# Kernel optimization log

Hardware: AMD Instinct MI355X
Metric: run time of the kernel (lower is better)

The kernel has to match this reference:

```python
import jax, jax.numpy as jnp
import numpy as np
from jax import lax

B, N, S = 16, 8192, 512
BASE_K = 16
MS_K = (8, 16, 24)


def _fps(xyz, npoint):
    # farthest point sampling; xyz [B,N,3] -> indices [B,npoint]
    b, n, _ = xyz.shape
    def body(carry, _):
        dists, far = carry
        c = jnp.take_along_axis(xyz, far[:, None, None], axis=1)  # [B,1,3]
        d = jnp.sum((xyz - c) ** 2, -1)
        dists = jnp.minimum(dists, d)
        return (dists, jnp.argmax(dists, -1).astype(jnp.int32)), far
    init = (jnp.full((b, n), 1e10, xyz.dtype), jnp.zeros((b,), jnp.int32))
    _, idx = lax.scan(body, init, None, length=npoint)
    return idx.swapaxes(0, 1)  # [B,npoint]


def _sqdist(a, b):
    # a [B,S,3], b [B,N,3] -> squared distances [B,S,N] (same topk order as cdist)
    return (jnp.sum(a * a, -1)[:, :, None] + jnp.sum(b * b, -1)[:, None, :]
            - 2.0 * jnp.einsum('bsc,bnc->bsn', a, b))


def _gather(pts, idx):
    # pts [B,N,C], idx [B,S,K] -> [B,S,K,C]
    b = pts.shape[0]
    return pts[jnp.arange(b)[:, None, None], idx]


def setup_inputs():
    key = jax.random.key(0)
    ks = jax.random.split(key, 6)
    s = 0.05
    return {
        'l0_xyz': jax.random.normal(ks[0], (B, 3, N), jnp.float32),
        'l0_points': jax.random.normal(ks[1], (B, 3, N), jnp.float32),
        'sa_W1': jax.random.normal(ks[2], (64, 6), jnp.float32) * s,
        'sa_b1': jnp.zeros((64,), jnp.float32),
        'sa_W2': jax.random.normal(ks[3], (128, 64), jnp.float32) * s,
        'sa_b2': jnp.zeros((128,), jnp.float32),
        'ms_W1': jax.random.normal(ks[4], (3, 64, 3), jnp.float32) * s,
        'ms_b1': jnp.zeros((3, 64), jnp.float32),
        'ms_W2': jax.random.normal(ks[5], (3, 128, 64), jnp.float32) * s,
        'ms_b2': jnp.zeros((3, 128), jnp.float32),
    }


def reference(l0_xyz, l0_points, sa_W1, sa_b1, sa_W2, sa_b2, ms_W1, ms_b1, ms_W2, ms_b2):
    xyz = l0_xyz.swapaxes(1, 2)     # [B,N,3]
    pts = l0_points.swapaxes(1, 2)  # [B,N,3]
    # --- PointNet_SA_Module_KNN: FPS + KNN grouping + shared MLP + max-pool ---
    fps_idx = _fps(lax.stop_gradient(xyz), S)                         # [B,S]
    new_xyz = jnp.take_along_axis(xyz, fps_idx[:, :, None], axis=1)  # [B,S,3]
    d = _sqdist(lax.stop_gradient(new_xyz), lax.stop_gradient(xyz))  # [B,S,N]
    _, knn_idx = lax.top_k(-d, BASE_K)                                # [B,S,K]
    g_xyz = _gather(xyz, knn_idx) - new_xyz[:, :, None]               # [B,S,K,3]
    g_pts = _gather(pts, knn_idx)                                     # [B,S,K,3]
    feat = jnp.concatenate([g_xyz, g_pts], -1)                        # [B,S,K,6]
    h = jax.nn.relu(jnp.einsum('bskc,oc->bsko', feat, sa_W1) + sa_b1)
    h = jnp.einsum('bsko,po->bskp', h, sa_W2) + sa_b2
    base_feat = jnp.max(h, axis=2)                                    # [B,S,128]
    keypoints = new_xyz.swapaxes(1, 2)                                # [B,3,S]
    # --- multi-scale: no_grad cdist, per-scale topk + rel-coord MLP + max-pool ---
    dist = _sqdist(lax.stop_gradient(new_xyz), lax.stop_gradient(xyz))  # [B,S,N]
    feats = [base_feat.swapaxes(1, 2)]                                  # [B,128,S]
    for i, k in enumerate(MS_K):
        k_eff = min(k, N)
        _, idx = lax.top_k(-dist, k_eff)                                # [B,S,k]
        rel = _gather(xyz, idx) - new_xyz[:, :, None]                   # [B,S,k,3]
        h = jax.nn.relu(jnp.einsum('bskc,oc->bsko', rel, ms_W1[i]) + ms_b1[i])
        h = jnp.einsum('bsko,po->bskp', h, ms_W2[i]) + ms_b2[i]
        feats.append(jnp.max(h, axis=2).swapaxes(1, 2))                 # [B,128,S]
    return keypoints, jnp.concatenate(feats, axis=1)                    # [B,3,S],[B,512,S]
```

## Files before the change

### kernel.cpp

```cpp
#include <hip/hip_runtime.h>

#define BB 16
#define NN 8192
#define SS 512
#define N3 (3 * NN)
#define KD 14

typedef unsigned short u16;
typedef unsigned int u32;
typedef unsigned long long u64;
typedef float v2f __attribute__((ext_vector_type(2)));

__device__ __forceinline__ v2f pk_add(v2f a, v2f b) {
  v2f r;
  asm("v_pk_add_f32 %0, %1, %2" : "=v"(r) : "v"(a), "v"(b));
  return r;
}
__device__ __forceinline__ v2f pk_mul(v2f a, v2f b) {
  v2f r;
  asm("v_pk_mul_f32 %0, %1, %2" : "=v"(r) : "v"(a), "v"(b));
  return r;
}

template <int CTRL>
__device__ __forceinline__ float dpp_maxf(float x) {
  int m = __builtin_amdgcn_update_dpp(0, __float_as_int(x), CTRL, 0xf, 0xf, false);
  return fmaxf(x, __int_as_float(m));
}
template <int CTRL>
__device__ __forceinline__ u32 dpp_maxu(u32 x) {
  u32 m = (u32)__builtin_amdgcn_update_dpp(0, (int)x, CTRL, 0xf, 0xf, false);
  return (x > m) ? x : m;
}

__global__ __attribute__((amdgpu_flat_work_group_size(256, 256),
                          amdgpu_waves_per_eu(1, 1)))
void k_fps(const float* __restrict__ xyz, float* __restrict__ out_kp) {
  __shared__ float sxyz[NN * 3];
  __shared__ int sIdx[SS];
  __shared__ u64 rkey[2][4];
  int b = blockIdx.x, t = threadIdx.x;
  const float* base = xyz + b * N3;
  v2f px[16], py[16], pz[16], dm[16];
#pragma unroll
  for (int j = 0; j < 16; ++j) {
    int n0 = j * 512 + t, n1 = n0 + 256;
    px[j] = v2f{base[n0], base[n1]};
    py[j] = v2f{base[NN + n0], base[NN + n1]};
    pz[j] = v2f{base[2 * NN + n0], base[2 * NN + n1]};
    dm[j] = v2f{1e10f, 1e10f};
    sxyz[n0 * 3 + 0] = px[j].x;
    sxyz[n0 * 3 + 1] = py[j].x;
    sxyz[n0 * 3 + 2] = pz[j].x;
    sxyz[n1 * 3 + 0] = px[j].y;
    sxyz[n1 * 3 + 1] = py[j].y;
    sxyz[n1 * 3 + 2] = pz[j].y;
  }
#pragma unroll
  for (int j = 0; j < 16; ++j) {
    asm volatile("" : "+v"(px[j]), "+v"(py[j]), "+v"(pz[j]));
  }
  float cx = base[0], cy = base[NN], cz = base[2 * NN];
  int far = 0;
  int lane = t & 63, w = t >> 6;
  u32 tb = (u32)(NN - t);
  for (int it = 0; it < SS; ++it) {
    if (t == 0) sIdx[it] = far;
    v2f ncx = v2f{-cx, -cx}, ncy = v2f{-cy, -cy}, ncz = v2f{-cz, -cz};
    float vmax = 0.0f;
#pragma unroll
    for (int j = 0; j < 16; ++j) {
      v2f dx = pk_add(px[j], ncx);
      v2f dy = pk_add(py[j], ncy);
      v2f dz = pk_add(pz[j], ncz);
      v2f xx = pk_mul(dx, dx);
      v2f yy = pk_mul(dy, dy);
      v2f s = pk_add(xx, yy);
      v2f zz = pk_mul(dz, dz);
      v2f d = pk_add(s, zz);
      float a0 = fminf(dm[j].x, d.x);
      float a1 = fminf(dm[j].y, d.y);
      dm[j].x = a0;
      dm[j].y = a1;
      vmax = fmaxf(vmax, fmaxf(a0, a1));
    }
    vmax = dpp_maxf<0x111>(vmax);
    vmax = dpp_maxf<0x112>(vmax);
    vmax = dpp_maxf<0x114>(vmax);
    vmax = dpp_maxf<0x118>(vmax);
    vmax = dpp_maxf<0x142>(vmax);
    vmax = dpp_maxf<0x143>(vmax);
    float wv = __int_as_float(__builtin_amdgcn_readlane(__float_as_int(vmax), 63));
    u32 cand = 0;
#pragma unroll
    for (int j = 15; j >= 0; --j) {
      u32 v1 = tb - (u32)(j * 512 + 256);
      u32 v0 = tb - (u32)(j * 512);
      cand = (dm[j].y == wv) ? v1 : cand;
      cand = (dm[j].x == wv) ? v0 : cand;
    }
    cand = dpp_maxu<0x111>(cand);
    cand = dpp_maxu<0x112>(cand);
    cand = dpp_maxu<0x114>(cand);
    cand = dpp_maxu<0x118>(cand);
    cand = dpp_maxu<0x142>(cand);
    cand = dpp_maxu<0x143>(cand);
    int pb = it & 1;
    if (lane == 63) rkey[pb][w] = ((u64)__float_as_uint(wv) << 32) | cand;
    __syncthreads();
    u64 k0 = rkey[pb][0], k1 = rkey[pb][1];
    u64 k2 = rkey[pb][2], k3 = rkey[pb][3];
    u64 k01 = (k0 > k1) ? k0 : k1;
    u64 k23 = (k2 > k3) ? k2 : k3;
    u64 kg = (k01 > k23) ? k01 : k23;
    far = NN - (int)(u32)(kg & 0xffffffffu);
    cx = sxyz[far * 3 + 0];
    cy = sxyz[far * 3 + 1];
    cz = sxyz[far * 3 + 2];
  }
  __syncthreads();
  for (int i = t; i < SS; i += 256) {
    int id = sIdx[i];
    out_kp[b * 1536 + i] = base[id];
    out_kp[b * 1536 + SS + i] = base[NN + id];
    out_kp[b * 1536 + 2 * SS + i] = base[2 * NN + id];
  }
}

__global__ __launch_bounds__(256) void k_knn(const float* __restrict__ xyz,
                                             const float* __restrict__ kp,
                                             u16* __restrict__ knn) {
  int t = threadIdx.x;
  int row = blockIdx.x * 4 + (t >> 6);
  int lane = t & 63;
  int b = row >> 9, s = row & (SS - 1);
  const float* base = xyz + b * N3;
  float ax = kp[b * 1536 + s];
  float ay = kp[b * 1536 + SS + s];
  float az = kp[b * 1536 + 2 * SS + s];
  float aw = __fadd_rn(__fadd_rn(__fmul_rn(ax, ax), __fmul_rn(ay, ay)), __fmul_rn(az, az));
  u64 arr[KD];
#pragma unroll
  for (int i = 0; i < KD; ++i) arr[i] = ~0ull;
  for (int c = 0; c < 128; ++c) {
    int n = c * 64 + lane;
    float qx = base[n], qy = base[NN + n], qz = base[2 * NN + n];
    float qw = __fadd_rn(__fadd_rn(__fmul_rn(qx, qx), __fmul_rn(qy, qy)), __fmul_rn(qz, qz));
    float dot = __fadd_rn(__fadd_rn(__fmul_rn(ax, qx), __fmul_rn(ay, qy)), __fmul_rn(az, qz));
    float d = __fsub_rn(__fadd_rn(aw, qw), __fmul_rn(2.0f, dot));
    u32 ub = __float_as_uint(d);
    ub ^= (ub & 0x80000000u) ? 0xFFFFFFFFu : 0x80000000u;
    u64 key = ((u64)ub << 32) | (u32)n;
    if (key < arr[KD - 1]) {
#pragma unroll
      for (int i = KD - 1; i >= 1; --i) {
        u64 am = arr[i - 1];
        arr[i] = (am > key) ? am : ((arr[i] > key) ? key : arr[i]);
      }
      if (arr[0] > key) arr[0] = key;
    }
  }
  u64 mine = 0;
  for (int it = 0; it < 24; ++it) {
    u64 m = arr[0];
#pragma unroll
    for (int off = 1; off < 64; off <<= 1) {
      u64 o = __shfl_xor(m, off, 64);
      m = (o < m) ? o : m;
    }
    if (lane == it) mine = m;
    if (arr[0] == m) {
#pragma unroll
      for (int i = 0; i < KD - 1; ++i) arr[i] = arr[i + 1];
      arr[KD - 1] = ~0ull;
    }
  }
  if (lane < 24) knn[row * 24 + lane] = (u16)(mine & 0xFFFFu);
}

__global__ __launch_bounds__(256) void k_base(
    const float* __restrict__ xyz, const float* __restrict__ pts,
    const float* __restrict__ kp, const u16* __restrict__ knn,
    const float* __restrict__ W1, const float* __restrict__ b1,
    const float* __restrict__ W2, const float* __restrict__ b2,
    float* __restrict__ out) {
  __shared__ float sW1T[6 * 64];
  __shared__ float sb1[64];
  __shared__ float sfeat[4][16 * 6];
  __shared__ float sh1[4][16 * 64];
  int t = threadIdx.x, lane = t & 63, w = t >> 6;
  int b = blockIdx.x >> 6, s0 = (blockIdx.x & 63) * 8;
  for (int i = t; i < 384; i += 256) {
    int o = i / 6, c = i - o * 6;
    sW1T[c * 64 + o] = W1[i];
  }
  if (t < 64) sb1[t] = b1[t];
  float wgtA[64], wgtB[64];
#pragma unroll
  for (int j = 0; j < 64; ++j) {
    wgtA[j] = W2[lane * 64 + j];
    wgtB[j] = W2[(lane + 64) * 64 + j];
  }
  float b2A = b2[lane], b2B = b2[lane + 64];
  __syncthreads();
  for (int g = 0; g < 2; ++g) {
    for (int i = t; i < 384; i += 256) {
      int rr = i / 96, rem = i - rr * 96, k = rem / 6, c = rem - k * 6;
      int s = s0 + g * 4 + rr, row = b * SS + s;
      int id = knn[row * 24 + k];
      float val;
      if (c < 3) {
        val = __fsub_rn(xyz[b * N3 + c * NN + id], kp[b * 1536 + c * SS + s]);
      } else {
        val = pts[b * N3 + (c - 3) * NN + id];
      }
      sfeat[rr][k * 6 + c] = val;
    }
    __syncthreads();
#pragma unroll
    for (int m = 0; m < 16; ++m) {
      int u = m * 256 + t;
      int rr = u >> 10, rem = u & 1023, k = rem >> 6, o = rem & 63;
      float acc = sb1[o];
#pragma unroll
      for (int c = 0; c < 6; ++c) acc = fmaf(sfeat[rr][k * 6 + c], sW1T[c * 64 + o], acc);
      sh1[rr][k * 64 + o] = fmaxf(acc, 0.f);
    }
    __syncthreads();
    float bestA = -1e30f, bestB = -1e30f;
#pragma unroll
    for (int k = 0; k < 16; ++k) {
      const float4* h4 = (const float4*)&sh1[w][k * 64];
      float a0 = 0.f, a1 = 0.f;
#pragma unroll
      for (int j = 0; j < 16; ++j) {
        float4 hv = h4[j];
        a0 = fmaf(hv.x, wgtA[4 * j], a0);
        a0 = fmaf(hv.y, wgtA[4 * j + 1], a0);
        a0 = fmaf(hv.z, wgtA[4 * j + 2], a0);
        a0 = fmaf(hv.w, wgtA[4 * j + 3], a0);
        a1 = fmaf(hv.x, wgtB[4 * j], a1);
        a1 = fmaf(hv.y, wgtB[4 * j + 1], a1);
        a1 = fmaf(hv.z, wgtB[4 * j + 2], a1);
        a1 = fmaf(hv.w, wgtB[4 * j + 3], a1);
      }
      bestA = fmaxf(bestA, a0);
      bestB = fmaxf(bestB, a1);
    }
    int s = s0 + g * 4 + w;
    out[24576 + b * 262144 + lane * 512 + s] = bestA + b2A;
    out[24576 + b * 262144 + (lane + 64) * 512 + s] = bestB + b2B;
    __syncthreads();
  }
}

__global__ __launch_bounds__(256) void k_ms(
    const float* __restrict__ xyz, const float* __restrict__ kp,
    const u16* __restrict__ knn, const float* __restrict__ msW1,
    const float* __restrict__ msb1, const float* __restrict__ msW2,
    const float* __restrict__ msb2, float* __restrict__ out) {
  int scale = blockIdx.y;
  int kk = 8 * (scale + 1);
  __shared__ float sW1T[3 * 64];
  __shared__ float sb1[64];
  __shared__ float sfeat[4][24 * 3];
  __shared__ float sh1[4][24 * 64];
  int t = threadIdx.x, lane = t & 63, w = t >> 6;
  int b = blockIdx.x >> 6, s0 = (blockIdx.x & 63) * 8;
  const float* W1s = msW1 + scale * 192;
  for (int i = t; i < 192; i += 256) {
    int o = i / 3, c = i - o * 3;
    sW1T[c * 64 + o] = W1s[i];
  }
  if (t < 64) sb1[t] = msb1[scale * 64 + t];
  float wgtA[64], wgtB[64];
#pragma unroll
  for (int j = 0; j < 64; ++j) {
    wgtA[j] = msW2[scale * 8192 + lane * 64 + j];
    wgtB[j] = msW2[scale * 8192 + (lane + 64) * 64 + j];
  }
  float b2A = msb2[scale * 128 + lane], b2B = msb2[scale * 128 + lane + 64];
  __syncthreads();
  int co = 128 * (scale + 1);
  for (int g = 0; g < 2; ++g) {
    int nfeat = 4 * kk * 3;
    for (int i = t; i < nfeat; i += 256) {
      int kk3 = kk * 3;
      int rr = i / kk3, rem = i - rr * kk3, k = rem / 3, c = rem - k * 3;
      int s = s0 + g * 4 + rr, row = b * SS + s;
      int id = knn[row * 24 + k];
      sfeat[rr][k * 3 + c] = __fsub_rn(xyz[b * N3 + c * NN + id], kp[b * 1536 + c * SS + s]);
    }
    __syncthreads();
    for (int rr = 0; rr < 4; ++rr) {
      for (int u = t; u < kk * 64; u += 256) {
        int k = u >> 6, o = u & 63;
        float acc = sb1[o];
        acc = fmaf(sfeat[rr][k * 3 + 0], sW1T[o], acc);
        acc = fmaf(sfeat[rr][k * 3 + 1], sW1T[64 + o], acc);
        acc = fmaf(sfeat[rr][k * 3 + 2], sW1T[128 + o], acc);
        sh1[rr][k * 64 + o] = fmaxf(acc, 0.f);
      }
    }
    __syncthreads();
    float bestA = -1e30f, bestB = -1e30f;
    for (int k = 0; k < kk; ++k) {
      const float4* h4 = (const float4*)&sh1[w][k * 64];
      float a0 = 0.f, a1 = 0.f;
#pragma unroll
      for (int j = 0; j < 16; ++j) {
        float4 hv = h4[j];
        a0 = fmaf(hv.x, wgtA[4 * j], a0);
        a0 = fmaf(hv.y, wgtA[4 * j + 1], a0);
        a0 = fmaf(hv.z, wgtA[4 * j + 2], a0);
        a0 = fmaf(hv.w, wgtA[4 * j + 3], a0);
        a1 = fmaf(hv.x, wgtB[4 * j], a1);
        a1 = fmaf(hv.y, wgtB[4 * j + 1], a1);
        a1 = fmaf(hv.z, wgtB[4 * j + 2], a1);
        a1 = fmaf(hv.w, wgtB[4 * j + 3], a1);
      }
      bestA = fmaxf(bestA, a0);
      bestB = fmaxf(bestB, a1);
    }
    int s = s0 + g * 4 + w;
    out[24576 + b * 262144 + (co + lane) * 512 + s] = bestA + b2A;
    out[24576 + b * 262144 + (co + lane + 64) * 512 + s] = bestB + b2B;
    __syncthreads();
  }
}

extern "C" void kernel_launch(void* const* d_in, const int* in_sizes, int n_in,
                              void* d_out, int out_size, void* d_ws, size_t ws_size,
                              hipStream_t stream) {
  const float* xyz = (const float*)d_in[0];
  const float* pts = (const float*)d_in[1];
  const float* sa_W1 = (const float*)d_in[2];
  const float* sa_b1 = (const float*)d_in[3];
  const float* sa_W2 = (const float*)d_in[4];
  const float* sa_b2 = (const float*)d_in[5];
  const float* ms_W1 = (const float*)d_in[6];
  const float* ms_b1 = (const float*)d_in[7];
  const float* ms_W2 = (const float*)d_in[8];
  const float* ms_b2 = (const float*)d_in[9];
  float* out = (float*)d_out;
  const float* kp = (const float*)d_out;

  u16* knn = (u16*)d_ws;

  k_fps<<<BB, 256, 0, stream>>>(xyz, out);
  k_knn<<<(BB * SS) / 4, 256, 0, stream>>>(xyz, kp, knn);
  k_base<<<BB * 64, 256, 0, stream>>>(xyz, pts, kp, knn, sa_W1, sa_b1, sa_W2, sa_b2, out);
  k_ms<<<dim3(BB * 64, 3), 256, 0, stream>>>(xyz, kp, knn, ms_W1, ms_b1, ms_W2, ms_b2, out);
}
```

Baseline: 1.031 ms.

## Fuse KNN, base MLP and multi-scale MLP into one kernel with packed FMA

New measurement: 1.829 ms. +77.5%, slower.

```diff
diff --git a/kernel.cpp b/kernel.cpp
--- a/kernel.cpp
+++ b/kernel.cpp
@@ -19,6 +19,11 @@
 __device__ __forceinline__ v2f pk_mul(v2f a, v2f b) {
   v2f r;
   asm("v_pk_mul_f32 %0, %1, %2" : "=v"(r) : "v"(a), "v"(b));
+  return r;
+}
+__device__ __forceinline__ v2f pk_fma(v2f a, v2f b, v2f c) {
+  v2f r;
+  asm("v_pk_fma_f32 %0, %1, %2, %3" : "=v"(r) : "v"(a), "v"(b), "v"(c));
   return r;
 }
 
@@ -127,205 +132,182 @@
   }
 }
 
-__global__ __launch_bounds__(256) void k_knn(const float* __restrict__ xyz,
-                                             const float* __restrict__ kp,
-                                             u16* __restrict__ knn) {
-  int t = threadIdx.x;
-  int row = blockIdx.x * 4 + (t >> 6);
-  int lane = t & 63;
-  int b = row >> 9, s = row & (SS - 1);
-  const float* base = xyz + b * N3;
-  float ax = kp[b * 1536 + s];
-  float ay = kp[b * 1536 + SS + s];
-  float az = kp[b * 1536 + 2 * SS + s];
-  float aw = __fadd_rn(__fadd_rn(__fmul_rn(ax, ax), __fmul_rn(ay, ay)), __fmul_rn(az, az));
-  u64 arr[KD];
-#pragma unroll
-  for (int i = 0; i < KD; ++i) arr[i] = ~0ull;
-  for (int c = 0; c < 128; ++c) {
-    int n = c * 64 + lane;
-    float qx = base[n], qy = base[NN + n], qz = base[2 * NN + n];
-    float qw = __fadd_rn(__fadd_rn(__fmul_rn(qx, qx), __fmul_rn(qy, qy)), __fmul_rn(qz, qz));
-    float dot = __fadd_rn(__fadd_rn(__fmul_rn(ax, qx), __fmul_rn(ay, qy)), __fmul_rn(az, qz));
-    float d = __fsub_rn(__fadd_rn(aw, qw), __fmul_rn(2.0f, dot));
-    u32 ub = __float_as_uint(d);
-    ub ^= (ub & 0x80000000u) ? 0xFFFFFFFFu : 0x80000000u;
-    u64 key = ((u64)ub << 32) | (u32)n;
-    if (key < arr[KD - 1]) {
-#pragma unroll
-      for (int i = KD - 1; i >= 1; --i) {
-        u64 am = arr[i - 1];
-        arr[i] = (am > key) ? am : ((arr[i] > key) ? key : arr[i]);
-      }
-      if (arr[0] > key) arr[0] = key;
-    }
-  }
-  u64 mine = 0;
-  for (int it = 0; it < 24; ++it) {
-    u64 m = arr[0];
-#pragma unroll
-    for (int off = 1; off < 64; off <<= 1) {
-      u64 o = __shfl_xor(m, off, 64);
-      m = (o < m) ? o : m;
-    }
-    if (lane == it) mine = m;
-    if (arr[0] == m) {
-#pragma unroll
-      for (int i = 0; i < KD - 1; ++i) arr[i] = arr[i + 1];
-      arr[KD - 1] = ~0ull;
-    }
-  }
-  if (lane < 24) knn[row * 24 + lane] = (u16)(mine & 0xFFFFu);
-}
-
-__global__ __launch_bounds__(256) void k_base(
-    const float* __restrict__ xyz, const float* __restrict__ pts,
-    const float* __restrict__ kp, const u16* __restrict__ knn,
-    const float* __restrict__ W1, const float* __restrict__ b1,
-    const float* __restrict__ W2, const float* __restrict__ b2,
-    float* __restrict__ out) {
+__global__ __attribute__((amdgpu_flat_work_group_size(256, 256),
+                          amdgpu_waves_per_eu(1, 1)))
+void k_tail(const float* __restrict__ xyz, const float* __restrict__ pts,
+            const float* __restrict__ kp, const float* __restrict__ W1,
+            const float* __restrict__ b1, const float* __restrict__ W2,
+            const float* __restrict__ b2, const float* __restrict__ msW1,
+            const float* __restrict__ msb1, const float* __restrict__ msW2,
+            const float* __restrict__ msb2, float* __restrict__ out) {
+  __shared__ u16 sknn[4][24];
   __shared__ float sW1T[6 * 64];
   __shared__ float sb1[64];
+  __shared__ float sW1m[3 * 64];
+  __shared__ float sb1m[64];
   __shared__ float sfeat[4][16 * 6];
-  __shared__ float sh1[4][16 * 64];
+  __shared__ float sh1[4][24 * 64];
   int t = threadIdx.x, lane = t & 63, w = t >> 6;
-  int b = blockIdx.x >> 6, s0 = (blockIdx.x & 63) * 8;
+  int row0 = blockIdx.x * 4;
+  int b = row0 >> 9;
+  int s0 = row0 & (SS - 1);
+  const float* base = xyz + b * N3;
+  const float* kpb = kp + b * 1536;
+  float* outb = out + 24576 + b * 262144;
+
   for (int i = t; i < 384; i += 256) {
     int o = i / 6, c = i - o * 6;
     sW1T[c * 64 + o] = W1[i];
   }
   if (t < 64) sb1[t] = b1[t];
-  float wgtA[64], wgtB[64];
-#pragma unroll
-  for (int j = 0; j < 64; ++j) {
-    wgtA[j] = W2[lane * 64 + j];
-    wgtB[j] = W2[(lane + 64) * 64 + j];
-  }
-  float b2A = b2[lane], b2B = b2[lane + 64];
+
+  {
+    int s = s0 + w;
+    float ax = kpb[s], ay = kpb[SS + s], az = kpb[2 * SS + s];
+    float aw = __fadd_rn(__fadd_rn(__fmul_rn(ax, ax), __fmul_rn(ay, ay)),
+                         __fmul_rn(az, az));
+    u64 arr[KD];
+#pragma unroll
+    for (int i = 0; i < KD; ++i) arr[i] = ~0ull;
+    for (int c = 0; c < 128; ++c) {
+      int n = c * 64 + lane;
+      float qx = base[n], qy = base[NN + n], qz = base[2 * NN + n];
+      float qw = __fadd_rn(__fadd_rn(__fmul_rn(qx, qx), __fmul_rn(qy, qy)),
+                           __fmul_rn(qz, qz));
+      float dot = __fadd_rn(__fadd_rn(__fmul_rn(ax, qx), __fmul_rn(ay, qy)),
+                            __fmul_rn(az, qz));
+      float d = __fsub_rn(__fadd_rn(aw, qw), __fmul_rn(2.0f, dot));
+      u32 ub = __float_as_uint(d);
+      ub ^= (ub & 0x80000000u) ? 0xFFFFFFFFu : 0x80000000u;
+      u64 key = ((u64)ub << 32) | (u32)n;
+      if (key < arr[KD - 1]) {
+#pragma unroll
+        for (int i = KD - 1; i >= 1; --i) {
+          u64 am = arr[i - 1];
+          arr[i] = (am > key) ? am : ((arr[i] > key) ? key : arr[i]);
+        }
+        if (arr[0] > key) arr[0] = key;
+      }
+    }
+    for (int it = 0; it < 24; ++it) {
+      u64 m = arr[0];
+#pragma unroll
+      for (int off = 1; off < 64; off <<= 1) {
+        u64 o = __shfl_xor(m, off, 64);
+        m = (o < m) ? o : m;
+      }
+      if (lane == it) sknn[w][it] = (u16)(m & 0xFFFFu);
+      if (arr[0] == m) {
+#pragma unroll
+        for (int i = 0; i < KD - 1; ++i) arr[i] = arr[i + 1];
+        arr[KD - 1] = ~0ull;
+      }
+    }
+  }
   __syncthreads();
-  for (int g = 0; g < 2; ++g) {
-    for (int i = t; i < 384; i += 256) {
-      int rr = i / 96, rem = i - rr * 96, k = rem / 6, c = rem - k * 6;
-      int s = s0 + g * 4 + rr, row = b * SS + s;
-      int id = knn[row * 24 + k];
-      float val;
-      if (c < 3) {
-        val = __fsub_rn(xyz[b * N3 + c * NN + id], kp[b * 1536 + c * SS + s]);
-      } else {
-        val = pts[b * N3 + (c - 3) * NN + id];
-      }
-      sfeat[rr][k * 6 + c] = val;
-    }
+
+  for (int i = t; i < 384; i += 256) {
+    int rr = i / 96, rem = i - rr * 96, k = rem / 6, c = rem - k * 6;
+    int s = s0 + rr;
+    int id = sknn[rr][k];
+    float val;
+    if (c < 3) {
+      val = __fsub_rn(base[c * NN + id], kpb[c * SS + s]);
+    } else {
+      val = pts[b * N3 + (c - 3) * NN + id];
+    }
+    sfeat[rr][k * 6 + c] = val;
+  }
+  __syncthreads();
+#pragma unroll
+  for (int m = 0; m < 16; ++m) {
+    int u = m * 256 + t;
+    int rr = u >> 10, rem = u & 1023, k = rem >> 6, o = rem & 63;
+    float acc = sb1[o];
+#pragma unroll
+    for (int c = 0; c < 6; ++c) acc = fmaf(sfeat[rr][k * 6 + c], sW1T[c * 64 + o], acc);
+    sh1[rr][k * 64 + o] = fmaxf(acc, 0.f);
+  }
+  __syncthreads();
+  {
+    const v2f* W2v = (const v2f*)W2;
+    v2f wA[32], wB[32];
+#pragma unroll
+    for (int j = 0; j < 32; ++j) {
+      wA[j] = W2v[lane * 32 + j];
+      wB[j] = W2v[(lane + 64) * 32 + j];
+    }
+    float bestA = -1e30f, bestB = -1e30f;
+#pragma unroll
+    for (int k = 0; k < 16; ++k) {
+      const v2f* h2 = (const v2f*)&sh1[w][k * 64];
+      v2f aA = v2f{0.f, 0.f}, aB = v2f{0.f, 0.f};
+#pragma unroll
+      for (int j = 0; j < 32; ++j) {
+        v2f hv = h2[j];
+        aA = pk_fma(hv, wA[j], aA);
+        aB = pk_fma(hv, wB[j], aB);
+      }
+      bestA = fmaxf(bestA, aA.x + aA.y);
+      bestB = fmaxf(bestB, aB.x + aB.y);
+    }
+    int s = s0 + w;
+    outb[lane * 512 + s] = bestA + b2[lane];
+    outb[(lane + 64) * 512 + s] = bestB + b2[lane + 64];
+  }
+
+  for (int scale = 0; scale < 3; ++scale) {
+    int kk = 8 * (scale + 1);
     __syncthreads();
-#pragma unroll
-    for (int m = 0; m < 16; ++m) {
-      int u = m * 256 + t;
-      int rr = u >> 10, rem = u & 1023, k = rem >> 6, o = rem & 63;
-      float acc = sb1[o];
-#pragma unroll
-      for (int c = 0; c < 6; ++c) acc = fmaf(sfeat[rr][k * 6 + c], sW1T[c * 64 + o], acc);
-      sh1[rr][k * 64 + o] = fmaxf(acc, 0.f);
-    }
-    __syncthreads();
-    float bestA = -1e30f, bestB = -1e30f;
-#pragma unroll
-    for (int k = 0; k < 16; ++k) {
-      const float4* h4 = (const float4*)&sh1[w][k * 64];
-      float a0 = 0.f, a1 = 0.f;
-#pragma unroll
-      for (int j = 0; j < 16; ++j) {
-        float4 hv = h4[j];
-        a0 = fmaf(hv.x, wgtA[4 * j], a0);
-        a0 = fmaf(hv.y, wgtA[4 * j + 1], a0);
-        a0 = fmaf(hv.z, wgtA[4 * j + 2], a0);
-        a0 = fmaf(hv.w, wgtA[4 * j + 3], a0);
-        a1 = fmaf(hv.x, wgtB[4 * j], a1);
-        a1 = fmaf(hv.y, wgtB[4 * j + 1], a1);
-        a1 = fmaf(hv.z, wgtB[4 * j + 2], a1);
-        a1 = fmaf(hv.w, wgtB[4 * j + 3], a1);
-      }
-      bestA = fmaxf(bestA, a0);
-      bestB = fmaxf(bestB, a1);
-    }
-    int s = s0 + g * 4 + w;
-    out[24576 + b * 262144 + lane * 512 + s] = bestA + b2A;
-    out[24576 + b * 262144 + (lane + 64) * 512 + s] = bestB + b2B;
-    __syncthreads();
-  }
-}
-
-__global__ __launch_bounds__(256) void k_ms(
-    const float* __restrict__ xyz, const float* __restrict__ kp,
-    const u16* __restrict__ knn, const float* __restrict__ msW1,
-    const float* __restrict__ msb1, const float* __restrict__ msW2,
-    const float* __restrict__ msb2, float* __restrict__ out) {
-  int scale = blockIdx.y;
-  int kk = 8 * (scale + 1);
-  __shared__ float sW1T[3 * 64];
-  __shared__ float sb1[64];
-  __shared__ float sfeat[4][24 * 3];
-  __shared__ float sh1[4][24 * 64];
-  int t = threadIdx.x, lane = t & 63, w = t >> 6;
-  int b = blockIdx.x >> 6, s0 = (blockIdx.x & 63) * 8;
-  const float* W1s = msW1 + scale * 192;
-  for (int i = t; i < 192; i += 256) {
-    int o = i / 3, c = i - o * 3;
-    sW1T[c * 64 + o] = W1s[i];
-  }
-  if (t < 64) sb1[t] = msb1[scale * 64 + t];
-  float wgtA[64], wgtB[64];
-#pragma unroll
-  for (int j = 0; j < 64; ++j) {
-    wgtA[j] = msW2[scale * 8192 + lane * 64 + j];
-    wgtB[j] = msW2[scale * 8192 + (lane + 64) * 64 + j];
-  }
-  float b2A = msb2[scale * 128 + lane], b2B = msb2[scale * 128 + lane + 64];
-  __syncthreads();
-  int co = 128 * (scale + 1);
-  for (int g = 0; g < 2; ++g) {
+    for (int i = t; i < 192; i += 256) {
+      int o = i / 3, c = i - o * 3;
+      sW1m[c * 64 + o] = msW1[scale * 192 + i];
+    }
+    if (t < 64) sb1m[t] = msb1[scale * 64 + t];
     int nfeat = 4 * kk * 3;
+    int kk3 = kk * 3;
     for (int i = t; i < nfeat; i += 256) {
-      int kk3 = kk * 3;
       int rr = i / kk3, rem = i - rr * kk3, k = rem / 3, c = rem - k * 3;
-      int s = s0 + g * 4 + rr, row = b * SS + s;
-      int id = knn[row * 24 + k];
-      sfeat[rr][k * 3 + c] = __fsub_rn(xyz[b * N3 + c * NN + id], kp[b * 1536 + c * SS + s]);
+      int s = s0 + rr;
+      int id = sknn[rr][k];
+      sfeat[rr][k * 3 + c] = __fsub_rn(base[c * NN + id], kpb[c * SS + s]);
     }
     __syncthreads();
     for (int rr = 0; rr < 4; ++rr) {
       for (int u = t; u < kk * 64; u += 256) {
         int k = u >> 6, o = u & 63;
-        float acc = sb1[o];
-        acc = fmaf(sfeat[rr][k * 3 + 0], sW1T[o], acc);
-        acc = fmaf(sfeat[rr][k * 3 + 1], sW1T[64 + o], acc);
-        acc = fmaf(sfeat[rr][k * 3 + 2], sW1T[128 + o], acc);
+        float acc = sb1m[o];
+        acc = fmaf(sfeat[rr][k * 3 + 0], sW1m[o], acc);
+        acc = fmaf(sfeat[rr][k * 3 + 1], sW1m[64 + o], acc);
+        acc = fmaf(sfeat[rr][k * 3 + 2], sW1m[128 + o], acc);
         sh1[rr][k * 64 + o] = fmaxf(acc, 0.f);
       }
     }
     __syncthreads();
+    const v2f* Wv = (const v2f*)(msW2 + scale * 8192);
+    v2f wA[32], wB[32];
+#pragma unroll
+    for (int j = 0; j < 32; ++j) {
+      wA[j] = Wv[lane * 32 + j];
+      wB[j] = Wv[(lane + 64) * 32 + j];
+    }
     float bestA = -1e30f, bestB = -1e30f;
     for (int k = 0; k < kk; ++k) {
-      const float4* h4 = (const float4*)&sh1[w][k * 64];
-      float a0 = 0.f, a1 = 0.f;
-#pragma unroll
-      for (int j = 0; j < 16; ++j) {
-        float4 hv = h4[j];
-        a0 = fmaf(hv.x, wgtA[4 * j], a0);
-        a0 = fmaf(hv.y, wgtA[4 * j + 1], a0);
-        a0 = fmaf(hv.z, wgtA[4 * j + 2], a0);
-        a0 = fmaf(hv.w, wgtA[4 * j + 3], a0);
-        a1 = fmaf(hv.x, wgtB[4 * j], a1);
-        a1 = fmaf(hv.y, wgtB[4 * j + 1], a1);
-        a1 = fmaf(hv.z, wgtB[4 * j + 2], a1);
-        a1 = fmaf(hv.w, wgtB[4 * j + 3], a1);
-      }
-      bestA = fmaxf(bestA, a0);
-      bestB = fmaxf(bestB, a1);
-    }
-    int s = s0 + g * 4 + w;
-    out[24576 + b * 262144 + (co + lane) * 512 + s] = bestA + b2A;
-    out[24576 + b * 262144 + (co + lane + 64) * 512 + s] = bestB + b2B;
-    __syncthreads();
+      const v2f* h2 = (const v2f*)&sh1[w][k * 64];
+      v2f aA = v2f{0.f, 0.f}, aB = v2f{0.f, 0.f};
+#pragma unroll
+      for (int j = 0; j < 32; ++j) {
+        v2f hv = h2[j];
+        aA = pk_fma(hv, wA[j], aA);
+        aB = pk_fma(hv, wB[j], aB);
+      }
+      bestA = fmaxf(bestA, aA.x + aA.y);
+      bestB = fmaxf(bestB, aB.x + aB.y);
+    }
+    int s = s0 + w;
+    int co = 128 * (scale + 1);
+    outb[(co + lane) * 512 + s] = bestA + msb2[scale * 128 + lane];
+    outb[(co + lane + 64) * 512 + s] = bestB + msb2[scale * 128 + lane + 64];
   }
 }
 
@@ -345,10 +327,7 @@
   float* out = (float*)d_out;
   const float* kp = (const float*)d_out;
 
-  u16* knn = (u16*)d_ws;
-
   k_fps<<<BB, 256, 0, stream>>>(xyz, out);
-  k_knn<<<(BB * SS) / 4, 256, 0, stream>>>(xyz, kp, knn);
-  k_base<<<BB * 64, 256, 0, stream>>>(xyz, pts, kp, knn, sa_W1, sa_b1, sa_W2, sa_b2, out);
-  k_ms<<<dim3(BB * 64, 3), 256, 0, stream>>>(xyz, kp, knn, ms_W1, ms_b1, ms_W2, ms_b2, out);
-}
+  k_tail<<<(BB * SS) / 4, 256, 0, stream>>>(xyz, pts, kp, sa_W1, sa_b1, sa_W2,
+                                            sa_b2, ms_W1, ms_b1, ms_W2, ms_b2, out);
+}
```
